# Kernel optimization log

Measured on AMD Instinct MI355X. Metric: run time of the kernel, lower is better.

## Reference

```python
import jax, jax.numpy as jnp
import numpy as np

B, N, D = 8, 4096, 512
NUM_CODES = 8192

def setup_inputs() -> dict:
    key = jax.random.key(0)
    kx, kc = jax.random.split(key)
    x = jax.random.normal(kx, (B, N, D), dtype=jnp.float32)
    codebook = jax.random.normal(kc, (NUM_CODES, D), dtype=jnp.float32)
    return {"x": x, "codebook": codebook}

def reference(x, codebook):
    # x: (B, N, D); codebook: (K, D)
    b = x.shape[0]
    flat = x.reshape(-1, x.shape[-1])  # (B*N, D)
    distances = (
        jnp.sum(flat * flat, axis=1, keepdims=True)
        + jnp.sum(codebook * codebook, axis=1)
        - 2.0 * flat @ codebook.T
    )
    codes = jnp.argmin(distances, axis=1).reshape(b, -1)  # (B, N) int
    return codes
```

## Files before the change

kernel.cpp:

```cpp
#include <hip/hip_runtime.h>
#include <hip/hip_bf16.h>
#include <hip/hip_fp16.h>


#define M_ROWS 32768
#define DDIM   512
#define KCODES 8192
#define NCAND  8

typedef unsigned long long u64;
typedef unsigned int u32;
typedef __attribute__((ext_vector_type(4))) float f32x4;
typedef __attribute__((ext_vector_type(8))) int v8i;

#define GL2LDS(gp, lp) __builtin_amdgcn_global_load_lds(                  \
    (const __attribute__((address_space(1))) void*)(gp),                  \
    (__attribute__((address_space(3))) void*)(lp), 16, 0, 0)

__device__ __forceinline__ u32 umin32(u32 a, u32 b) { return a < b ? a : b; }
__device__ __forceinline__ u32 umax32(u32 a, u32 b) { return a > b ? a : b; }
__device__ __forceinline__ u64 umin64(u64 a, u64 b) { return a < b ? a : b; }
__device__ __forceinline__ u32 umin3(u32 a, u32 b, u32 c) {
  return umin32(umin32(a, b), c);
}
__device__ __forceinline__ u32 med3u(u32 a, u32 b, u32 c) {
  u32 d;
  asm("v_med3_u32 %0, %1, %2, %3" : "=v"(d) : "v"(a), "v"(b), "v"(c));
  return d;
}

__device__ __forceinline__ u32 fsort(float s) {
  u32 fb = __float_as_uint(s);
  return fb ^ (u32)(((int)fb >> 31) | 0x80000000);
}

__device__ __forceinline__ uint2 pk8_fp8(float4 v0, float4 v1) {
  int lo = 0, hi = 0;
  lo = __builtin_amdgcn_cvt_pk_fp8_f32(v0.x, v0.y, lo, false);
  lo = __builtin_amdgcn_cvt_pk_fp8_f32(v0.z, v0.w, lo, true);
  hi = __builtin_amdgcn_cvt_pk_fp8_f32(v1.x, v1.y, hi, false);
  hi = __builtin_amdgcn_cvt_pk_fp8_f32(v1.z, v1.w, hi, true);
  return (uint2){(u32)lo, (u32)hi};
}

__global__ __launch_bounds__(256) void conv_codebook_kernel(
    const float* __restrict__ cb, unsigned char* __restrict__ ch8,
    float* __restrict__ cnh) {
  int wave = (blockIdx.x * 256 + threadIdx.x) >> 6;
  int lane = threadIdx.x & 63;
  if (wave >= KCODES) return;
  const float* src = cb + (size_t)wave * DDIM + lane * 8;
  float4 v0 = *(const float4*)(src);
  float4 v1 = *(const float4*)(src + 4);
  *(uint2*)(ch8 + (size_t)wave * DDIM + lane * 8) = pk8_fp8(v0, v1);
  float ss = v0.x*v0.x + v0.y*v0.y + v0.z*v0.z + v0.w*v0.w
           + v1.x*v1.x + v1.y*v1.y + v1.z*v1.z + v1.w*v1.w;
#pragma unroll
  for (int off = 32; off; off >>= 1) ss += __shfl_xor(ss, off);
  if (lane == 0) cnh[wave] = 0.5f * ss;
}

__global__ __launch_bounds__(256) void conv_x_kernel(
    const float* __restrict__ x, unsigned char* __restrict__ xh8) {
  size_t i = ((size_t)blockIdx.x * 256 + threadIdx.x) * 8;
  float4 v0 = *(const float4*)(x + i);
  float4 v1 = *(const float4*)(x + i + 4);
  *(uint2*)(xh8 + i) = pk8_fp8(v0, v1);
}

__device__ __forceinline__ v8i ld_frag(const char* L, int row, int g) {
  const int base = row * 128;
  const int sl = ((g * 2) ^ (row & 7)) * 16;
  int4 lo = *(const int4*)&L[base + sl];
  int4 hi = *(const int4*)&L[base + (sl ^ 16)];
  v8i r;
  r[0] = lo.x; r[1] = lo.y; r[2] = lo.z; r[3] = lo.w;
  r[4] = hi.x; r[5] = hi.y; r[6] = hi.z; r[7] = hi.w;
  return r;
}

__global__ __launch_bounds__(256) void coarse_kernel(
    const unsigned char* __restrict__ xh8, const unsigned char* __restrict__ ch8,
    const float* __restrict__ cnh, uint4* __restrict__ part) {
  __shared__ __align__(16) char smem[65536];
  uint4* tab = (uint4*)smem;

  const int tid  = threadIdx.x;
  const int lane = tid & 63;
  const int wid  = tid >> 6;
  const int wm   = wid >> 1, wn = wid & 1;
  const int g    = lane >> 4, l16 = lane & 15;

  const int xcd  = blockIdx.x & 7;
  const int lid  = blockIdx.x >> 3;
  const int nblk = lid >> 5;
  const int mblk = (xcd << 5) | (lid & 31);
  const int row0 = mblk * 128;
  const int col0 = nblk * 128;

  const int a_ = lane >> 3, b_ = lane & 7;
  const size_t gsrc = (size_t)a_ * DDIM + ((b_ ^ a_) << 4);
  const unsigned char* abase = xh8 + (size_t)row0 * DDIM + gsrc;
  const unsigned char* bbase = ch8 + (size_t)col0 * DDIM + gsrc;

#define STAGE(cc, buf) do {                                               \
    char* sa_ = smem + (buf) * 32768;                                     \
    _Pragma("unroll")                                                     \
    for (int j = 0; j < 4; ++j) {                                         \
      const int I_ = wid * 4 + j;                                         \
      const size_t off_ = (size_t)(I_ * 8) * DDIM + (size_t)(cc) * 128;   \
      GL2LDS(abase + off_, sa_ + I_ * 1024);                              \
      GL2LDS(bbase + off_, sa_ + 16384 + I_ * 1024);                      \
    }                                                                     \
  } while (0)

  u32 codev[4];
  float cn[4];
#pragma unroll
  for (int tn = 0; tn < 4; ++tn) {
    codev[tn] = (u32)(col0 + wn * 64 + tn * 16 + l16);
    cn[tn] = cnh[codev[tn]];
  }

  f32x4 acc[4][4];
#pragma unroll
  for (int tm = 0; tm < 4; ++tm)
#pragma unroll
    for (int tn = 0; tn < 4; ++tn) acc[tm][tn] = (f32x4){0.f, 0.f, 0.f, 0.f};

  STAGE(0, 0);
  __syncthreads();

#pragma unroll
  for (int c = 0; c < 4; ++c) {
    if (c < 3) STAGE(c + 1, (c + 1) & 1);
    const char* aL = smem + (c & 1) * 32768;
    const char* bL = aL + 16384;

    v8i af[4];
#pragma unroll
    for (int t = 0; t < 4; ++t)
      af[t] = ld_frag(aL, wm * 64 + t * 16 + l16, g);
#pragma unroll
    for (int tn = 0; tn < 4; ++tn) {
      v8i bf = ld_frag(bL, wn * 64 + tn * 16 + l16, g);
#pragma unroll
      for (int tm = 0; tm < 4; ++tm)
        acc[tm][tn] = __builtin_amdgcn_mfma_scale_f32_16x16x128_f8f6f4(
            af[tm], bf, acc[tm][tn],
            0, 0,
            0, 0x7F7F7F7F,
            0, 0x7F7F7F7F);
    }
    __syncthreads();
  }

  u32 k1[16], k2[16], k3[16];
#pragma unroll
  for (int tm = 0; tm < 4; ++tm)
#pragma unroll
    for (int r = 0; r < 4; ++r) {
      const int sl = tm * 4 + r;
      u32 key[4];
#pragma unroll
      for (int tn = 0; tn < 4; ++tn) {
        float s = cn[tn] - acc[tm][tn][r];
        key[tn] = (__float_as_uint(s) & 0xFFFFE000u) | codev[tn];
      }
      u32 a1 = umin32(key[0], key[1]);
      u32 a2 = umax32(key[0], key[1]);
      u32 a3 = ~0u;
      {
        u32 lo = umin32(key[2], key[3]), hi = umax32(key[2], key[3]);
        u32 m  = umax32(a1, lo);
        a1 = umin32(a1, lo);
        u32 b3 = med3u(a2, m, hi);
        a2 = umin3(a2, m, hi);
        a3 = umin32(a3, b3);
      }
      k1[sl] = a1; k2[sl] = a2; k3[sl] = a3;
    }

  u32 m1 = ~0u, m2 = ~0u, m3 = ~0u;
#pragma unroll
  for (int p = 0; p < 2; ++p) {
    __syncthreads();
    if (wn == p) {
#pragma unroll
      for (int tm = 0; tm < 4; ++tm)
#pragma unroll
        for (int r = 0; r < 4; ++r) {
          const int row = wm * 64 + tm * 16 + g * 4 + r;
          const int sl = tm * 4 + r;
          tab[row * 17 + l16] = (uint4){k1[sl], k2[sl], k3[sl], 0u};
        }
    }
    __syncthreads();
    if (tid < 128) {
#pragma unroll
      for (int e = 0; e < 16; ++e) {
        uint4 v = tab[tid * 17 + e];
        u32 a = umax32(m1, v.x);
        m1 = umin32(m1, v.x);
        u32 b = med3u(m2, a, v.y);
        m2 = umin3(m2, a, v.y);
        m3 = umin3(m3, b, v.z);
      }
    }
  }

  if (tid < 128)
    part[(size_t)nblk * M_ROWS + row0 + tid] = (uint4){m1, m2, m3, 0u};
#undef STAGE
}

__global__ __launch_bounds__(256) void merge_kernel(
    const uint4* __restrict__ part, int* __restrict__ cand) {
  const int row = blockIdx.x * 256 + threadIdx.x;
  u32 k[NCAND];
#pragma unroll
  for (int i = 0; i < NCAND; ++i) k[i] = ~0u;
  for (int nb = 0; nb < KCODES / 128; ++nb) {
    uint4 e = part[(size_t)nb * M_ROWS + row];
    u32 t = e.x;
#pragma unroll
    for (int i = 0; i < NCAND; ++i) { u32 mx = umax32(k[i], t); k[i] = umin32(k[i], t); t = mx; }
    t = e.y;
#pragma unroll
    for (int i = 0; i < NCAND; ++i) { u32 mx = umax32(k[i], t); k[i] = umin32(k[i], t); t = mx; }
    t = e.z;
#pragma unroll
    for (int i = 0; i < NCAND; ++i) { u32 mx = umax32(k[i], t); k[i] = umin32(k[i], t); t = mx; }
  }
#pragma unroll
  for (int i = 0; i < NCAND; ++i)
    cand[row * NCAND + i] = (int)(k[i] & 0x1FFFu);
}

__global__ __launch_bounds__(256) void rescore_kernel(
    const float* __restrict__ x, const float* __restrict__ cb,
    const float* __restrict__ cnh, const int* __restrict__ cand,
    int* __restrict__ out) {
  int wave = (blockIdx.x * 256 + threadIdx.x) >> 6;
  int lane = threadIdx.x & 63;
  if (wave >= M_ROWS) return;
  int idx[NCAND];
#pragma unroll
  for (int j = 0; j < NCAND; ++j) idx[j] = cand[wave * NCAND + j];

  const float* xr = x + (size_t)wave * DDIM + lane * 8;
  float4 x0 = *(const float4*)(xr);
  float4 x1 = *(const float4*)(xr + 4);

  float d[NCAND];
#pragma unroll
  for (int j = 0; j < NCAND; ++j) {
    const float* c = cb + (size_t)idx[j] * DDIM + lane * 8;
    float4 a0 = *(const float4*)(c);
    float4 a1 = *(const float4*)(c + 4);
    d[j] = x0.x*a0.x + x0.y*a0.y + x0.z*a0.z + x0.w*a0.w
         + x1.x*a1.x + x1.y*a1.y + x1.z*a1.z + x1.w*a1.w;
  }
#pragma unroll
  for (int off = 32; off; off >>= 1)
#pragma unroll
    for (int j = 0; j < NCAND; ++j) d[j] += __shfl_xor(d[j], off);

  if (lane == 0) {
    u64 best = ~0ull;
#pragma unroll
    for (int j = 0; j < NCAND; ++j) {
      float s = cnh[idx[j]] - d[j];
      u64 key = ((u64)fsort(s) << 32) | (u32)idx[j];
      best = umin64(best, key);
    }
    out[wave] = (int)(u32)best;
  }
}

extern "C" void kernel_launch(void* const* d_in, const int* in_sizes, int n_in,
                              void* d_out, int out_size, void* d_ws, size_t ws_size,
                              hipStream_t stream) {
  const float* x  = (const float*)d_in[0];
  const float* cb = (const float*)d_in[1];
  int* out = (int*)d_out;

  char* ws = (char*)d_ws;
  unsigned char* ch8  = (unsigned char*)(ws);
  unsigned char* xh8  = (unsigned char*)(ws + (size_t)4 * 1024 * 1024);
  float*         cnh  = (float*)(ws + (size_t)20 * 1024 * 1024);
  int*           cand = (int*)(ws + (size_t)20 * 1024 * 1024 + 32 * 1024);
  uint4*         part = (uint4*)(ws + (size_t)22 * 1024 * 1024);

  conv_codebook_kernel<<<KCODES / 4, 256, 0, stream>>>(cb, ch8, cnh);
  conv_x_kernel<<<(M_ROWS * DDIM) / (256 * 8), 256, 0, stream>>>(x, xh8);
  coarse_kernel<<<(M_ROWS / 128) * (KCODES / 128), 256, 0, stream>>>(xh8, ch8, cnh, part);
  merge_kernel<<<M_ROWS / 256, 256, 0, stream>>>(part, cand);
  rescore_kernel<<<M_ROWS / 4, 256, 0, stream>>>(x, cb, cnh, cand, out);
}
```

Baseline: 384.1 us.

## Split coarse GEMM block into eight waves with smaller per-wave tiles

The coarse fp8 MFMA kernel now runs 512 threads per block (2x4 waves), so each wave owns a 64x32 output tile instead of 64x64. Accumulator and key registers are halved, which allows higher occupancy, and the staging loads are spread over more waves. Fragment addresses are precomputed outside the loop. The cross-wave top-3 merge now takes four passes over LDS with two keys per slot, which adds barriers and reduction work in exchange.

New measurement: 373.4 us. 2.8% less time.

```diff
diff --git a/kernel.cpp b/kernel.cpp
--- a/kernel.cpp
+++ b/kernel.cpp
@@ -68,27 +68,16 @@
   *(uint2*)(xh8 + i) = pk8_fp8(v0, v1);
 }
 
-__device__ __forceinline__ v8i ld_frag(const char* L, int row, int g) {
-  const int base = row * 128;
-  const int sl = ((g * 2) ^ (row & 7)) * 16;
-  int4 lo = *(const int4*)&L[base + sl];
-  int4 hi = *(const int4*)&L[base + (sl ^ 16)];
-  v8i r;
-  r[0] = lo.x; r[1] = lo.y; r[2] = lo.z; r[3] = lo.w;
-  r[4] = hi.x; r[5] = hi.y; r[6] = hi.z; r[7] = hi.w;
-  return r;
-}
-
-__global__ __launch_bounds__(256) void coarse_kernel(
+__global__ __launch_bounds__(512, 4) void coarse_kernel(
     const unsigned char* __restrict__ xh8, const unsigned char* __restrict__ ch8,
     const float* __restrict__ cnh, uint4* __restrict__ part) {
   __shared__ __align__(16) char smem[65536];
-  uint4* tab = (uint4*)smem;
+  uint2* tab = (uint2*)smem;
 
   const int tid  = threadIdx.x;
   const int lane = tid & 63;
   const int wid  = tid >> 6;
-  const int wm   = wid >> 1, wn = wid & 1;
+  const int wm   = wid >> 2, wn = wid & 3;
   const int g    = lane >> 4, l16 = lane & 15;
 
   const int xcd  = blockIdx.x & 7;
@@ -103,30 +92,35 @@
   const unsigned char* abase = xh8 + (size_t)row0 * DDIM + gsrc;
   const unsigned char* bbase = ch8 + (size_t)col0 * DDIM + gsrc;
 
+  const int sl0 = (((g * 2) ^ (l16 & 7)) << 4);
+  const int slX = sl0 ^ 16;
+  const int aoff = (wm * 64 + l16) * 128;
+  const int boff = (wn * 32 + l16) * 128;
+
 #define STAGE(cc, buf) do {                                               \
     char* sa_ = smem + (buf) * 32768;                                     \
     _Pragma("unroll")                                                     \
-    for (int j = 0; j < 4; ++j) {                                         \
-      const int I_ = wid * 4 + j;                                         \
+    for (int j = 0; j < 2; ++j) {                                         \
+      const int I_ = wid * 2 + j;                                         \
       const size_t off_ = (size_t)(I_ * 8) * DDIM + (size_t)(cc) * 128;   \
       GL2LDS(abase + off_, sa_ + I_ * 1024);                              \
       GL2LDS(bbase + off_, sa_ + 16384 + I_ * 1024);                      \
     }                                                                     \
   } while (0)
 
-  u32 codev[4];
-  float cn[4];
-#pragma unroll
-  for (int tn = 0; tn < 4; ++tn) {
-    codev[tn] = (u32)(col0 + wn * 64 + tn * 16 + l16);
+  u32 codev[2];
+  float cn[2];
+#pragma unroll
+  for (int tn = 0; tn < 2; ++tn) {
+    codev[tn] = (u32)(col0 + wn * 32 + tn * 16 + l16);
     cn[tn] = cnh[codev[tn]];
   }
 
-  f32x4 acc[4][4];
+  f32x4 acc[4][2];
 #pragma unroll
   for (int tm = 0; tm < 4; ++tm)
 #pragma unroll
-    for (int tn = 0; tn < 4; ++tn) acc[tm][tn] = (f32x4){0.f, 0.f, 0.f, 0.f};
+    for (int tn = 0; tn < 2; ++tn) acc[tm][tn] = (f32x4){0.f, 0.f, 0.f, 0.f};
 
   STAGE(0, 0);
   __syncthreads();
@@ -136,14 +130,26 @@
     if (c < 3) STAGE(c + 1, (c + 1) & 1);
     const char* aL = smem + (c & 1) * 32768;
     const char* bL = aL + 16384;
+    const char* paL = aL + aoff + sl0;
+    const char* paH = aL + aoff + slX;
+    const char* pbL = bL + boff + sl0;
+    const char* pbH = bL + boff + slX;
 
     v8i af[4];
 #pragma unroll
-    for (int t = 0; t < 4; ++t)
-      af[t] = ld_frag(aL, wm * 64 + t * 16 + l16, g);
-#pragma unroll
-    for (int tn = 0; tn < 4; ++tn) {
-      v8i bf = ld_frag(bL, wn * 64 + tn * 16 + l16, g);
+    for (int t = 0; t < 4; ++t) {
+      int4 lo = *(const int4*)(paL + t * 2048);
+      int4 hi = *(const int4*)(paH + t * 2048);
+      af[t][0] = lo.x; af[t][1] = lo.y; af[t][2] = lo.z; af[t][3] = lo.w;
+      af[t][4] = hi.x; af[t][5] = hi.y; af[t][6] = hi.z; af[t][7] = hi.w;
+    }
+#pragma unroll
+    for (int tn = 0; tn < 2; ++tn) {
+      int4 lo = *(const int4*)(pbL + tn * 2048);
+      int4 hi = *(const int4*)(pbH + tn * 2048);
+      v8i bf;
+      bf[0] = lo.x; bf[1] = lo.y; bf[2] = lo.z; bf[3] = lo.w;
+      bf[4] = hi.x; bf[5] = hi.y; bf[6] = hi.z; bf[7] = hi.w;
 #pragma unroll
       for (int tm = 0; tm < 4; ++tm)
         acc[tm][tn] = __builtin_amdgcn_mfma_scale_f32_16x16x128_f8f6f4(
@@ -155,35 +161,23 @@
     __syncthreads();
   }
 
-  u32 k1[16], k2[16], k3[16];
+  u32 k1[16], k2[16];
 #pragma unroll
   for (int tm = 0; tm < 4; ++tm)
 #pragma unroll
     for (int r = 0; r < 4; ++r) {
       const int sl = tm * 4 + r;
-      u32 key[4];
-#pragma unroll
-      for (int tn = 0; tn < 4; ++tn) {
-        float s = cn[tn] - acc[tm][tn][r];
-        key[tn] = (__float_as_uint(s) & 0xFFFFE000u) | codev[tn];
-      }
-      u32 a1 = umin32(key[0], key[1]);
-      u32 a2 = umax32(key[0], key[1]);
-      u32 a3 = ~0u;
-      {
-        u32 lo = umin32(key[2], key[3]), hi = umax32(key[2], key[3]);
-        u32 m  = umax32(a1, lo);
-        a1 = umin32(a1, lo);
-        u32 b3 = med3u(a2, m, hi);
-        a2 = umin3(a2, m, hi);
-        a3 = umin32(a3, b3);
-      }
-      k1[sl] = a1; k2[sl] = a2; k3[sl] = a3;
+      float s0 = cn[0] - acc[tm][0][r];
+      float s1 = cn[1] - acc[tm][1][r];
+      u32 key0 = (__float_as_uint(s0) & 0xFFFFE000u) | codev[0];
+      u32 key1 = (__float_as_uint(s1) & 0xFFFFE000u) | codev[1];
+      k1[sl] = umin32(key0, key1);
+      k2[sl] = umax32(key0, key1);
     }
 
   u32 m1 = ~0u, m2 = ~0u, m3 = ~0u;
 #pragma unroll
-  for (int p = 0; p < 2; ++p) {
+  for (int p = 0; p < 4; ++p) {
     __syncthreads();
     if (wn == p) {
 #pragma unroll
@@ -192,19 +186,19 @@
         for (int r = 0; r < 4; ++r) {
           const int row = wm * 64 + tm * 16 + g * 4 + r;
           const int sl = tm * 4 + r;
-          tab[row * 17 + l16] = (uint4){k1[sl], k2[sl], k3[sl], 0u};
+          tab[row * 17 + l16] = (uint2){k1[sl], k2[sl]};
         }
     }
     __syncthreads();
     if (tid < 128) {
 #pragma unroll
       for (int e = 0; e < 16; ++e) {
-        uint4 v = tab[tid * 17 + e];
+        uint2 v = tab[tid * 17 + e];
         u32 a = umax32(m1, v.x);
         m1 = umin32(m1, v.x);
         u32 b = med3u(m2, a, v.y);
         m2 = umin3(m2, a, v.y);
-        m3 = umin3(m3, b, v.z);
+        m3 = umin32(m3, b);
       }
     }
   }
@@ -294,7 +288,7 @@
 
   conv_codebook_kernel<<<KCODES / 4, 256, 0, stream>>>(cb, ch8, cnh);
   conv_x_kernel<<<(M_ROWS * DDIM) / (256 * 8), 256, 0, stream>>>(x, xh8);
-  coarse_kernel<<<(M_ROWS / 128) * (KCODES / 128), 256, 0, stream>>>(xh8, ch8, cnh, part);
+  coarse_kernel<<<(M_ROWS / 128) * (KCODES / 128), 512, 0, stream>>>(xh8, ch8, cnh, part);
   merge_kernel<<<M_ROWS / 256, 256, 0, stream>>>(part, cand);
   rescore_kernel<<<M_ROWS / 4, 256, 0, stream>>>(x, cb, cnh, cand, out);
 }
```
